# Performance work log

Measured on AMD Instinct MI355X. Metric: run time of the kernel, lower is better.

Reference implementation:

```python
import jax, jax.numpy as jnp
import numpy as np

HEADS = 8
DIM_HEAD = 128
LN_EPS = 1e-5


def setup_inputs() -> dict:
    key = jax.random.key(0)
    ks = jax.random.split(key, 4)
    N, M, C, V, T = 64, 2, 64, 15, 256
    dim = C * V              # 960
    inner = HEADS * DIM_HEAD # 1024
    return {
        "x": jax.random.normal(ks[0], (N, M, C, V, T), dtype=jnp.float32),
        "ln_g": jnp.ones((dim,), jnp.float32),
        "ln_b": jnp.zeros((dim,), jnp.float32),
        "w_qkv": jax.random.normal(ks[1], (dim, 3 * inner), dtype=jnp.float32) * (dim ** -0.5),
        "w_out": jax.random.normal(ks[2], (inner, dim), dtype=jnp.float32) * (inner ** -0.5),
        "b_out": jnp.zeros((dim,), jnp.float32),
        "w_lin": jax.random.normal(ks[3], (T, T), dtype=jnp.float32) * (T ** -0.5),
        "b_lin": jnp.zeros((T,), jnp.float32),
    }


def reference(x, ln_g, ln_b, w_qkv, w_out, b_out, w_lin, b_lin):
    N, M, C, V, T = x.shape
    dim = C * V
    # [N, M, C, V, T] -> [N*M, T, C*V]
    xs = jnp.transpose(x, (0, 1, 4, 2, 3)).reshape(N * M, T, dim)

    # PreNorm (LayerNorm over last dim)
    mu = jnp.mean(xs, axis=-1, keepdims=True)
    var = jnp.mean(jnp.square(xs - mu), axis=-1, keepdims=True)
    xn = (xs - mu) * jax.lax.rsqrt(var + LN_EPS) * ln_g + ln_b

    # Attention
    qkv = xn @ w_qkv  # [NM, T, 3*inner]
    q, k, v = jnp.split(qkv, 3, axis=-1)
    def to_heads(t):
        return jnp.transpose(t.reshape(N * M, T, HEADS, DIM_HEAD), (0, 2, 1, 3))
    q, k, v = to_heads(q), to_heads(k), to_heads(v)  # [NM, H, T, D]
    scale = DIM_HEAD ** -0.5
    dots = jnp.einsum('nhid,nhjd->nhij', q, k) * scale
    attn = jax.nn.softmax(dots, axis=-1)
    out = jnp.einsum('nhij,nhjd->nhid', attn, v)
    out = jnp.transpose(out, (0, 2, 1, 3)).reshape(N * M, T, HEADS * DIM_HEAD)
    out = out @ w_out + b_out

    # Residual
    xs = out + xs

    # back to [N, M, C, V, T], then Linear over T + tanh
    x2 = jnp.transpose(xs.reshape(N, M, T, C, V), (0, 1, 3, 4, 2))
    y = jnp.tanh(x2 @ w_lin.T + b_lin)
    return y
```

## Files before the change

kernel.cpp:

```cpp
#include <hip/hip_runtime.h>

typedef unsigned short ushort;
using short8 = __attribute__((ext_vector_type(8))) short;
using f32x4  = __attribute__((ext_vector_type(4))) float;
using i32x4  = __attribute__((ext_vector_type(4))) int;
using us4    = __attribute__((ext_vector_type(4))) ushort;

static __device__ __forceinline__ float bf2f(ushort u) {
  union { unsigned int i; float f; } x; x.i = ((unsigned int)u) << 16; return x.f;
}
static __device__ __forceinline__ ushort f2bf(float f) {
  union { float f; unsigned int i; } x; x.f = f;
  unsigned int u = x.i;
  unsigned int r = u + 0x7fffu + ((u >> 16) & 1u);
  return (ushort)(r >> 16);
}

#define GLOAD16(gp, lp)                                                   \
  __builtin_amdgcn_global_load_lds(                                      \
      (const __attribute__((address_space(1))) void*)(gp),               \
      (__attribute__((address_space(3))) void*)(lp), 16, 0, 0)

__global__ __launch_bounds__(256) void wtrans_kernel(const float* __restrict__ in,
                                                     ushort* __restrict__ out,
                                                     int R, int C) {
  __shared__ float sl[32][33];
  int tx = threadIdx.x & 31, ty = threadIdx.x >> 5;
  int c0 = blockIdx.x * 32, r0 = blockIdx.y * 32;
#pragma unroll
  for (int s = 0; s < 4; s++) {
    int r = r0 + ty + s * 8;
    int c = c0 + tx;
    sl[ty + s * 8][tx] = (c < C) ? in[(size_t)r * C + c] : 0.f;
  }
  __syncthreads();
#pragma unroll
  for (int s = 0; s < 4; s++) {
    int c = c0 + ty + s * 8;
    int r = r0 + tx;
    out[(size_t)c * R + r] = f2bf(sl[tx][ty + s * 8]);
  }
}

__global__ void wsplit_kernel(const float* __restrict__ in, ushort* __restrict__ hi,
                              ushort* __restrict__ lo, int n) {
  int i = blockIdx.x * 256 + threadIdx.x;
  if (i < n) {
    float v = in[i];
    ushort h = f2bf(v);
    hi[i] = h;
    lo[i] = f2bf(v - bf2f(h));
  }
}

__global__ __launch_bounds__(256) void ln_fused_kernel(const float* __restrict__ x,
                                                       const float* __restrict__ g,
                                                       const float* __restrict__ b,
                                                       ushort* __restrict__ xn) {
  __shared__ float sl[960][20];
  __shared__ float smean[16], srstd[16];
  int tid = threadIdx.x;
  int nm = blockIdx.y;
  int t0 = blockIdx.x * 16;

  int r0 = tid >> 2, c4 = (tid & 3) * 4;
#pragma unroll
  for (int it = 0; it < 15; it++) {
    int r = it * 64 + r0;
    float4 v = *(const float4*)&x[((size_t)nm * 960 + r) * 256 + t0 + c4];
    *(float4*)&sl[r][c4] = v;
  }
  __syncthreads();

  int tg = tid >> 4, lt = tid & 15;
  float s = 0.f, ss = 0.f;
#pragma unroll 4
  for (int k = 0; k < 60; k++) {
    float v = sl[lt + k * 16][tg];
    s += v; ss += v * v;
  }
#pragma unroll
  for (int d = 1; d < 16; d <<= 1) {
    s += __shfl_xor(s, d, 64);
    ss += __shfl_xor(ss, d, 64);
  }
  if (lt == 0) {
    float mean = s * (1.f / 960.f);
    float var = ss * (1.f / 960.f) - mean * mean;
    smean[tg] = mean;
    srstd[tg] = rsqrtf(var + 1e-5f);
  }
  __syncthreads();

  float gg[4], bb[4];
#pragma unroll
  for (int c = 0; c < 4; c++) {
    int col = c * 256 + tid;
    if (col < 960) { gg[c] = g[col]; bb[c] = b[col]; }
  }
#pragma unroll
  for (int t = 0; t < 16; t++) {
    float mean = smean[t], rstd = srstd[t];
#pragma unroll
    for (int c = 0; c < 4; c++) {
      int col = c * 256 + tid;
      if (col < 960)
        xn[((size_t)nm * 256 + t0 + t) * 960 + col] =
            f2bf((sl[col][t] - mean) * rstd * gg[c] + bb[c]);
    }
  }
}

template <int MODE>
__global__ __launch_bounds__(512, 2) void gemm256(
    const ushort* __restrict__ A, int lda, const ushort* __restrict__ BT, int ldb, int nkt,
    const ushort* __restrict__ Alo, const ushort* __restrict__ Blo,
    ushort* __restrict__ o0, ushort* __restrict__ o1, ushort* __restrict__ o2,
    const float* __restrict__ bias, float* __restrict__ fout) {
  __shared__ char smem[131072];
  int tid = threadIdx.x;
  int l = tid & 63, w = tid >> 6;
  int wr = w >> 2, wc = w & 3;
  int lr = l & 15, lg = l >> 4;
  int cb = blockIdx.x * 256, rb = blockIdx.y * 256;

  int srow = tid >> 2;
  int scol = ((tid & 3) ^ ((tid >> 3) & 3)) * 8;

  int swz = (lg ^ ((lr >> 1) & 3)) << 4;
  const char* ArdB = smem + (wr * 128 + lr) * 64 + swz;
  const char* BrdB = smem + 65536 + (wc * 64 + lr) * 64 + swz;

  auto stage_half = [&](int kt, int kk, int isB) {
    const ushort* P; int ld; int k0;
    if (MODE == 2) {
      int seg = kt >> 2; k0 = (kt & 3) * 64 + kk * 32;
      P = isB ? ((seg == 1) ? Blo : BT) : ((seg == 2) ? Alo : A);
      ld = 256;
    } else {
      P = isB ? BT : A; ld = isB ? ldb : lda; k0 = kt * 64 + kk * 32;
    }
    const ushort* gp = P + (size_t)((isB ? cb : rb) + srow) * ld + k0 + scol;
    char* dst = smem + isB * 65536 + (kt & 1) * 32768 + kk * 16384 + tid * 16;
    GLOAD16(gp, dst);
    GLOAD16(gp + (size_t)128 * ld, dst + 8192);
  };

  f32x4 acc[8][4];
#pragma unroll
  for (int i = 0; i < 8; i++)
#pragma unroll
    for (int j = 0; j < 4; j++) acc[i][j] = (f32x4){0.f, 0.f, 0.f, 0.f};

  stage_half(0, 0, 0); stage_half(0, 0, 1); stage_half(0, 1, 0); stage_half(0, 1, 1);
  asm volatile("s_waitcnt vmcnt(4)" ::: "memory");
  __builtin_amdgcn_s_barrier();

  for (int t = 0; t < nkt; t++) {
    const char* Ard = ArdB + (t & 1) * 32768;
    const char* Brd = BrdB + (t & 1) * 32768;
    bool st = (t + 1 < nkt);
    short8 a[4], b[4];

#pragma unroll
    for (int j = 0; j < 4; j++) b[j] = *(const short8*)(Brd + j * 1024);
#pragma unroll
    for (int i = 0; i < 4; i++) a[i] = *(const short8*)(Ard + i * 1024);
    if (st) stage_half(t + 1, 0, 0);
    __builtin_amdgcn_s_barrier();
    __builtin_amdgcn_s_setprio(1);
#pragma unroll
    for (int i = 0; i < 4; i++)
#pragma unroll
      for (int j = 0; j < 4; j++)
        acc[i][j] = __builtin_amdgcn_mfma_f32_16x16x32_bf16(a[i], b[j], acc[i][j], 0, 0, 0);
    __builtin_amdgcn_s_setprio(0);
    __builtin_amdgcn_s_barrier();

#pragma unroll
    for (int i = 0; i < 4; i++) a[i] = *(const short8*)(Ard + (4 + i) * 1024);
    if (st) stage_half(t + 1, 0, 1);
    __builtin_amdgcn_s_barrier();
    __builtin_amdgcn_s_setprio(1);
#pragma unroll
    for (int i = 0; i < 4; i++)
#pragma unroll
      for (int j = 0; j < 4; j++)
        acc[4 + i][j] = __builtin_amdgcn_mfma_f32_16x16x32_bf16(a[i], b[j], acc[4 + i][j], 0, 0, 0);
    __builtin_amdgcn_s_setprio(0);
    if (st) asm volatile("s_waitcnt vmcnt(4)" ::: "memory");
    else    asm volatile("s_waitcnt vmcnt(0)" ::: "memory");
    __builtin_amdgcn_s_barrier();

#pragma unroll
    for (int j = 0; j < 4; j++) b[j] = *(const short8*)(Brd + 16384 + j * 1024);
#pragma unroll
    for (int i = 0; i < 4; i++) a[i] = *(const short8*)(Ard + 16384 + i * 1024);
    if (st) stage_half(t + 1, 1, 0);
    __builtin_amdgcn_s_barrier();
    __builtin_amdgcn_s_setprio(1);
#pragma unroll
    for (int i = 0; i < 4; i++)
#pragma unroll
      for (int j = 0; j < 4; j++)
        acc[i][j] = __builtin_amdgcn_mfma_f32_16x16x32_bf16(a[i], b[j], acc[i][j], 0, 0, 0);
    __builtin_amdgcn_s_setprio(0);
    __builtin_amdgcn_s_barrier();

#pragma unroll
    for (int i = 0; i < 4; i++) a[i] = *(const short8*)(Ard + 16384 + (4 + i) * 1024);
    if (st) stage_half(t + 1, 1, 1);
    __builtin_amdgcn_s_barrier();
    __builtin_amdgcn_s_setprio(1);
#pragma unroll
    for (int i = 0; i < 4; i++)
#pragma unroll
      for (int j = 0; j < 4; j++)
        acc[4 + i][j] = __builtin_amdgcn_mfma_f32_16x16x32_bf16(a[i], b[j], acc[4 + i][j], 0, 0, 0);
    __builtin_amdgcn_s_setprio(0);
    if (st) asm volatile("s_waitcnt vmcnt(4)" ::: "memory");
    else    asm volatile("s_waitcnt vmcnt(0)" ::: "memory");
    __builtin_amdgcn_s_barrier();
  }

  int row0 = rb + wr * 128, col0 = cb + wc * 64;
  if (MODE == 0) {
    int nm = rb >> 8;
    int which = cb >> 10;
#pragma unroll
    for (int i = 0; i < 8; i++)
#pragma unroll
      for (int j = 0; j < 4; j++) {
        f32x4 v = acc[i][j];
        int col = col0 + j * 16 + lr;
        int cl = col & 1023;
        int h = cl >> 7, d = cl & 127;
        int nmh = nm * 8 + h;
        int t0 = wr * 128 + i * 16 + lg * 4;
        if (which == 2) {
          us4 pk;
          pk.x = f2bf(v[0]); pk.y = f2bf(v[1]); pk.z = f2bf(v[2]); pk.w = f2bf(v[3]);
          *(us4*)&o2[((size_t)nmh * 128 + d) * 256 + t0] = pk;
        } else if (which == 0) {
#pragma unroll
          for (int r = 0; r < 4; r++)
            o0[((size_t)nmh * 256 + t0 + r) * 128 + d] = f2bf(v[r] * 0.08838834764831845f);
        } else {
#pragma unroll
          for (int r = 0; r < 4; r++)
            o1[((size_t)nmh * 256 + t0 + r) * 128 + d] = f2bf(v[r]);
        }
      }
  } else if (MODE == 1) {
#pragma unroll
    for (int i = 0; i < 8; i++)
#pragma unroll
      for (int j = 0; j < 4; j++) {
        f32x4 v = acc[i][j];
        int col = col0 + j * 16 + lr;
        float bb = (col < 960) ? bias[col] : 0.f;
#pragma unroll
        for (int r = 0; r < 4; r++) {
          int row = row0 + i * 16 + lg * 4 + r;
          o0[(size_t)row * 1024 + col] = f2bf(v[r] + bb);
        }
      }
  } else {
#pragma unroll
    for (int i = 0; i < 8; i++)
#pragma unroll
      for (int j = 0; j < 4; j++) {
        f32x4 v = acc[i][j];
        int col = col0 + j * 16 + lr;
        float bb = bias[col];
#pragma unroll
        for (int r = 0; r < 4; r++) {
          int row = row0 + i * 16 + lg * 4 + r;
          fout[(size_t)row * 256 + col] = tanhf(v[r] + bb);
        }
      }
  }
}

__global__ __launch_bounds__(256) void attn_kernel(const ushort* __restrict__ q,
                                                   const ushort* __restrict__ kb,
                                                   const ushort* __restrict__ vT,
                                                   ushort* __restrict__ ao) {
  __shared__ ushort KVs[128 * 72];
  __shared__ ushort Ps[64 * 264];
  int tid = threadIdx.x;
  int l = tid & 63, w = tid >> 6;
  int lr = l & 15, lg = l >> 4;
  int qb = blockIdx.x;
  int nmh = blockIdx.y;

  short8 aq[4];
  {
    const ushort* qp = q + ((size_t)nmh * 256 + qb * 64 + w * 16 + lr) * 128 + lg * 8;
#pragma unroll
    for (int kk = 0; kk < 4; kk++) aq[kk] = *(const short8*)(qp + kk * 32);
  }

  f32x4 s_acc[16];
#pragma unroll
  for (int f = 0; f < 16; f++) s_acc[f] = (f32x4){0.f, 0.f, 0.f, 0.f};

  for (int ct = 0; ct < 4; ct++) {
    __syncthreads();
#pragma unroll
    for (int u = 0; u < 4; u++) {
      int i = tid + u * 256;
      int r = i >> 4, c = i & 15;
      *(i32x4*)&KVs[r * 136 + c * 8] =
          *(const i32x4*)(kb + ((size_t)nmh * 256 + ct * 64 + r) * 128 + c * 8);
    }
    __syncthreads();
#pragma unroll
    for (int j = 0; j < 4; j++) {
      short8 bk[4];
#pragma unroll
      for (int kk = 0; kk < 4; kk++)
        bk[kk] = *(const short8*)&KVs[(j * 16 + lr) * 136 + kk * 32 + lg * 8];
#pragma unroll
      for (int kk = 0; kk < 4; kk++)
        s_acc[ct * 4 + j] =
            __builtin_amdgcn_mfma_f32_16x16x32_bf16(aq[kk], bk[kk], s_acc[ct * 4 + j], 0, 0, 0);
    }
  }

  float m[4] = {-1e30f, -1e30f, -1e30f, -1e30f};
#pragma unroll
  for (int f = 0; f < 16; f++)
#pragma unroll
    for (int r = 0; r < 4; r++) m[r] = fmaxf(m[r], s_acc[f][r]);
#pragma unroll
  for (int dd = 1; dd < 16; dd <<= 1)
#pragma unroll
    for (int r = 0; r < 4; r++) m[r] = fmaxf(m[r], __shfl_xor(m[r], dd, 64));
  float sum[4] = {0.f, 0.f, 0.f, 0.f};
#pragma unroll
  for (int f = 0; f < 16; f++)
#pragma unroll
    for (int r = 0; r < 4; r++) {
      float p = __expf(s_acc[f][r] - m[r]);
      s_acc[f][r] = p;
      sum[r] += p;
    }
#pragma unroll
  for (int dd = 1; dd < 16; dd <<= 1)
#pragma unroll
    for (int r = 0; r < 4; r++) sum[r] += __shfl_xor(sum[r], dd, 64);
  float rs[4];
#pragma unroll
  for (int r = 0; r < 4; r++) rs[r] = 1.f / sum[r];

#pragma unroll
  for (int f = 0; f < 16; f++)
#pragma unroll
    for (int r = 0; r < 4; r++)
      Ps[(w * 16 + lg * 4 + r) * 264 + f * 16 + lr] = f2bf(s_acc[f][r]);

  f32x4 o_acc[8];
#pragma unroll
  for (int j = 0; j < 8; j++) o_acc[j] = (f32x4){0.f, 0.f, 0.f, 0.f};

  for (int ct = 0; ct < 4; ct++) {
    __syncthreads();
#pragma unroll
    for (int u = 0; u < 4; u++) {
      int i = tid + u * 256;
      int r = i >> 3, c = i & 7;
      *(i32x4*)&KVs[r * 72 + c * 8] =
          *(const i32x4*)(vT + ((size_t)nmh * 128 + r) * 256 + ct * 64 + c * 8);
    }
    __syncthreads();
#pragma unroll
    for (int kk = 0; kk < 2; kk++) {
      short8 ap = *(const short8*)&Ps[(w * 16 + lr) * 264 + ct * 64 + kk * 32 + lg * 8];
#pragma unroll
      for (int j = 0; j < 8; j++) {
        short8 bv = *(const short8*)&KVs[(j * 16 + lr) * 72 + kk * 32 + lg * 8];
        o_acc[j] = __builtin_amdgcn_mfma_f32_16x16x32_bf16(ap, bv, o_acc[j], 0, 0, 0);
      }
    }
  }

  int nm = nmh >> 3, h = nmh & 7;
  int trow0 = qb * 64 + w * 16;
#pragma unroll
  for (int j = 0; j < 8; j++)
#pragma unroll
    for (int r = 0; r < 4; r++) {
      int t = trow0 + lg * 4 + r;
      int d = h * 128 + j * 16 + lr;
      ao[((size_t)nm * 256 + t) * 1024 + d] = f2bf(o_acc[j][r] * rs[r]);
    }
}

__global__ __launch_bounds__(256) void x2split_kernel(const float* __restrict__ x,
                                                      const ushort* __restrict__ proj,
                                                      ushort* __restrict__ hi,
                                                      ushort* __restrict__ lo) {
  __shared__ ushort sl[64][65];
  int nm = blockIdx.y;
  int tb = blockIdx.x & 3, cvb = blockIdx.x >> 2;
  int t0 = tb * 64, cv0 = cvb * 64;
  int tx = threadIdx.x & 63, ty = threadIdx.x >> 6;
#pragma unroll
  for (int s = 0; s < 16; s++) {
    int r = ty + s * 4;
    sl[r][tx] = proj[((size_t)nm * 256 + t0 + r) * 1024 + cv0 + tx];
  }
  __syncthreads();
#pragma unroll
  for (int s = 0; s < 16; s++) {
    int cvl = ty + s * 4;
    size_t R = (size_t)nm * 960 + cv0 + cvl;
    float v = x[R * 256 + t0 + tx] + bf2f(sl[tx][cvl]);
    ushort h = f2bf(v);
    hi[R * 256 + t0 + tx] = h;
    lo[R * 256 + t0 + tx] = f2bf(v - bf2f(h));
  }
}

extern "C" void kernel_launch(void* const* d_in, const int* in_sizes, int n_in,
                              void* d_out, int out_size, void* d_ws, size_t ws_size,
                              hipStream_t stream) {
  const float* x = (const float*)d_in[0];
  const float* ln_g = (const float*)d_in[1];
  const float* ln_b = (const float*)d_in[2];
  const float* w_qkv = (const float*)d_in[3];
  const float* w_out = (const float*)d_in[4];
  const float* b_out = (const float*)d_in[5];
  const float* w_lin = (const float*)d_in[6];
  const float* b_lin = (const float*)d_in[7];
  float* out = (float*)d_out;

  char* ws = (char*)d_ws;
  size_t off = 0;
  auto alloc = [&](size_t bytes) -> void* {
    void* p = ws + off;
    off = (off + bytes + 255) & ~(size_t)255;
    return p;
  };

  ushort* wqkvT = (ushort*)alloc((size_t)3072 * 960 * 2);
  ushort* woutT = (ushort*)alloc((size_t)1024 * 1024 * 2);
  ushort* whi   = (ushort*)alloc((size_t)65536 * 2);
  ushort* wlo   = (ushort*)alloc((size_t)65536 * 2);
  ushort* xn    = (ushort*)alloc((size_t)32768 * 960 * 2);
  ushort* qbuf  = (ushort*)alloc((size_t)1024 * 256 * 128 * 2);
  ushort* kbuf  = (ushort*)alloc((size_t)1024 * 256 * 128 * 2);
  ushort* vTbuf = (ushort*)alloc((size_t)1024 * 256 * 128 * 2);
  ushort* attnout = (ushort*)alloc((size_t)32768 * 1024 * 2);
  ushort* proj = qbuf;
  ushort* x2hi = kbuf;
  ushort* x2lo = vTbuf;

  wtrans_kernel<<<dim3(96, 30), 256, 0, stream>>>(w_qkv, wqkvT, 960, 3072);
  wtrans_kernel<<<dim3(32, 32), 256, 0, stream>>>(w_out, woutT, 1024, 960);
  wsplit_kernel<<<dim3(256), 256, 0, stream>>>(w_lin, whi, wlo, 65536);

  ln_fused_kernel<<<dim3(16, 128), 256, 0, stream>>>(x, ln_g, ln_b, xn);

  gemm256<0><<<dim3(12, 128), 512, 0, stream>>>(xn, 960, wqkvT, 960, 15, nullptr, nullptr,
                                                qbuf, kbuf, vTbuf, nullptr, nullptr);
  attn_kernel<<<dim3(4, 1024), 256, 0, stream>>>(qbuf, kbuf, vTbuf, attnout);
  gemm256<1><<<dim3(4, 128), 512, 0, stream>>>(attnout, 1024, woutT, 1024, 16, nullptr, nullptr,
                                               proj, nullptr, nullptr, b_out, nullptr);
  x2split_kernel<<<dim3(60, 128), 256, 0, stream>>>(x, proj, x2hi, x2lo);
  gemm256<2><<<dim3(1, 480), 512, 0, stream>>>(x2hi, 256, whi, 256, 12, x2lo, wlo,
                                               nullptr, nullptr, nullptr, b_lin, out);
}
```

Before: 683.7 us.

## Process whole head per attention block and store projection transposed

The attention kernel now gives one 512-thread block a whole head. It loads all of K and V^T once into 128KB of swizzled LDS with async global-to-LDS loads, and each wave handles 32 query rows. This removes the 4x redundant K/V loads and the repeated barriers of the old per-64-row blocks. The out-projection GEMM epilogue writes its result transposed ([nm][cv][t]) as packed 4-element stores, so the residual/split kernel becomes a simple vectorized elementwise pass with no LDS transpose. The cost is fewer resident blocks per CU (large LDS), plus reliance on correct vmcnt waits and swizzle indexing.

```diff
diff --git a/kernel.cpp b/kernel.cpp
--- a/kernel.cpp
+++ b/kernel.cpp
@@ -252,6 +252,7 @@
         }
       }
   } else if (MODE == 1) {
+    int nm = rb >> 8;
 #pragma unroll
     for (int i = 0; i < 8; i++)
 #pragma unroll
@@ -259,11 +260,11 @@
         f32x4 v = acc[i][j];
         int col = col0 + j * 16 + lr;
         float bb = (col < 960) ? bias[col] : 0.f;
-#pragma unroll
-        for (int r = 0; r < 4; r++) {
-          int row = row0 + i * 16 + lg * 4 + r;
-          o0[(size_t)row * 1024 + col] = f2bf(v[r] + bb);
-        }
+        int t0 = wr * 128 + i * 16 + lg * 4;
+        us4 pk;
+        pk.x = f2bf(v[0] + bb); pk.y = f2bf(v[1] + bb);
+        pk.z = f2bf(v[2] + bb); pk.w = f2bf(v[3] + bb);
+        *(us4*)&o0[((size_t)nm * 1024 + col) * 256 + t0] = pk;
       }
   } else {
 #pragma unroll
@@ -282,145 +283,177 @@
   }
 }
 
-__global__ __launch_bounds__(256) void attn_kernel(const ushort* __restrict__ q,
-                                                   const ushort* __restrict__ kb,
-                                                   const ushort* __restrict__ vT,
-                                                   ushort* __restrict__ ao) {
-  __shared__ ushort KVs[128 * 72];
-  __shared__ ushort Ps[64 * 264];
+__global__ __launch_bounds__(512, 2) void attn2_kernel(const ushort* __restrict__ q,
+                                                       const ushort* __restrict__ kb,
+                                                       const ushort* __restrict__ vT,
+                                                       ushort* __restrict__ ao) {
+  __shared__ char smem[131072];
   int tid = threadIdx.x;
   int l = tid & 63, w = tid >> 6;
   int lr = l & 15, lg = l >> 4;
-  int qb = blockIdx.x;
-  int nmh = blockIdx.y;
-
-  short8 aq[4];
+  int nmh = blockIdx.x;
+
+  const ushort* kbase = kb + (size_t)nmh * 32768;
+  const ushort* vbase = vT + (size_t)nmh * 32768;
+
+#pragma unroll
+  for (int u = 0; u < 8; u++) {
+    int row = u * 32 + w * 4 + (l >> 4);
+    int slot = l & 15;
+    GLOAD16(kbase + row * 128 + ((slot ^ (row & 7)) * 8), smem + u * 8192 + w * 1024);
+  }
+  short8 aq[2][4];
   {
-    const ushort* qp = q + ((size_t)nmh * 256 + qb * 64 + w * 16 + lr) * 128 + lg * 8;
-#pragma unroll
-    for (int kk = 0; kk < 4; kk++) aq[kk] = *(const short8*)(qp + kk * 32);
-  }
-
-  f32x4 s_acc[16];
-#pragma unroll
-  for (int f = 0; f < 16; f++) s_acc[f] = (f32x4){0.f, 0.f, 0.f, 0.f};
-
+    const ushort* qp = q + (size_t)nmh * 32768 + (size_t)(w * 32 + lr) * 128 + lg * 8;
+#pragma unroll
+    for (int i = 0; i < 2; i++)
+#pragma unroll
+      for (int kk = 0; kk < 4; kk++) aq[i][kk] = *(const short8*)(qp + i * 2048 + kk * 32);
+  }
+#pragma unroll
+  for (int u = 0; u < 8; u++) {
+    int row = u * 16 + w * 2 + (l >> 5);
+    int slot = l & 31;
+    GLOAD16(vbase + row * 256 + ((slot ^ (row & 7)) * 8),
+            smem + 65536 + u * 8192 + w * 1024);
+  }
+  asm volatile("s_waitcnt vmcnt(8)" ::: "memory");
+  __builtin_amdgcn_s_barrier();
+
+  f32x4 s_acc[2][16];
+#pragma unroll
+  for (int i = 0; i < 2; i++)
+#pragma unroll
+    for (int j = 0; j < 16; j++) s_acc[i][j] = (f32x4){0.f, 0.f, 0.f, 0.f};
+#pragma unroll
+  for (int j = 0; j < 16; j++) {
+    short8 bk[4];
+#pragma unroll
+    for (int kk = 0; kk < 4; kk++)
+      bk[kk] = *(const short8*)(smem + (j * 16 + lr) * 256 + (((kk * 4 + lg) ^ (lr & 7)) << 4));
+#pragma unroll
+    for (int i = 0; i < 2; i++)
+#pragma unroll
+      for (int kk = 0; kk < 4; kk++)
+        s_acc[i][j] = __builtin_amdgcn_mfma_f32_16x16x32_bf16(aq[i][kk], bk[kk], s_acc[i][j], 0, 0, 0);
+  }
+
+  float m[2][4], sum[2][4], rs[2][4];
+#pragma unroll
+  for (int i = 0; i < 2; i++)
+#pragma unroll
+    for (int r = 0; r < 4; r++) m[i][r] = -1e30f;
+#pragma unroll
+  for (int i = 0; i < 2; i++)
+#pragma unroll
+    for (int j = 0; j < 16; j++)
+#pragma unroll
+      for (int r = 0; r < 4; r++) m[i][r] = fmaxf(m[i][r], s_acc[i][j][r]);
+#pragma unroll
+  for (int d = 1; d < 16; d <<= 1)
+#pragma unroll
+    for (int i = 0; i < 2; i++)
+#pragma unroll
+      for (int r = 0; r < 4; r++) m[i][r] = fmaxf(m[i][r], __shfl_xor(m[i][r], d, 64));
+#pragma unroll
+  for (int i = 0; i < 2; i++)
+#pragma unroll
+    for (int r = 0; r < 4; r++) sum[i][r] = 0.f;
+#pragma unroll
+  for (int i = 0; i < 2; i++)
+#pragma unroll
+    for (int j = 0; j < 16; j++)
+#pragma unroll
+      for (int r = 0; r < 4; r++) {
+        float p = __expf(s_acc[i][j][r] - m[i][r]);
+        s_acc[i][j][r] = p;
+        sum[i][r] += p;
+      }
+#pragma unroll
+  for (int d = 1; d < 16; d <<= 1)
+#pragma unroll
+    for (int i = 0; i < 2; i++)
+#pragma unroll
+      for (int r = 0; r < 4; r++) sum[i][r] += __shfl_xor(sum[i][r], d, 64);
+#pragma unroll
+  for (int i = 0; i < 2; i++)
+#pragma unroll
+    for (int r = 0; r < 4; r++) rs[i][r] = 1.f / sum[i][r];
+
+  __builtin_amdgcn_s_barrier();
+  asm volatile("s_waitcnt vmcnt(0)" ::: "memory");
+
+  char* Pb = smem + w * 4608;
+  f32x4 o_acc[2][8];
+#pragma unroll
+  for (int i = 0; i < 2; i++)
+#pragma unroll
+    for (int j = 0; j < 8; j++) o_acc[i][j] = (f32x4){0.f, 0.f, 0.f, 0.f};
+
+#pragma unroll
   for (int ct = 0; ct < 4; ct++) {
-    __syncthreads();
-#pragma unroll
-    for (int u = 0; u < 4; u++) {
-      int i = tid + u * 256;
-      int r = i >> 4, c = i & 15;
-      *(i32x4*)&KVs[r * 136 + c * 8] =
-          *(const i32x4*)(kb + ((size_t)nmh * 256 + ct * 64 + r) * 128 + c * 8);
+#pragma unroll
+    for (int i = 0; i < 2; i++)
+#pragma unroll
+      for (int jj = 0; jj < 4; jj++)
+#pragma unroll
+        for (int r = 0; r < 4; r++)
+          *(ushort*)(Pb + (i * 16 + lg * 4 + r) * 144 + (jj * 16 + lr) * 2) =
+              f2bf(s_acc[i][ct * 4 + jj][r]);
+    short8 pa[2][2];
+#pragma unroll
+    for (int i = 0; i < 2; i++)
+#pragma unroll
+      for (int kk = 0; kk < 2; kk++)
+        pa[i][kk] = *(const short8*)(Pb + (i * 16 + lr) * 144 + kk * 64 + lg * 16);
+#pragma unroll
+    for (int j = 0; j < 8; j++) {
+      short8 bv[2];
+#pragma unroll
+      for (int kk = 0; kk < 2; kk++)
+        bv[kk] = *(const short8*)(smem + 65536 + (j * 16 + lr) * 512 +
+                                  (((ct * 8 + kk * 4 + lg) ^ (lr & 7)) << 4));
+#pragma unroll
+      for (int i = 0; i < 2; i++)
+#pragma unroll
+        for (int kk = 0; kk < 2; kk++)
+          o_acc[i][j] = __builtin_amdgcn_mfma_f32_16x16x32_bf16(pa[i][kk], bv[kk], o_acc[i][j], 0, 0, 0);
     }
-    __syncthreads();
-#pragma unroll
-    for (int j = 0; j < 4; j++) {
-      short8 bk[4];
-#pragma unroll
-      for (int kk = 0; kk < 4; kk++)
-        bk[kk] = *(const short8*)&KVs[(j * 16 + lr) * 136 + kk * 32 + lg * 8];
-#pragma unroll
-      for (int kk = 0; kk < 4; kk++)
-        s_acc[ct * 4 + j] =
-            __builtin_amdgcn_mfma_f32_16x16x32_bf16(aq[kk], bk[kk], s_acc[ct * 4 + j], 0, 0, 0);
-    }
-  }
-
-  float m[4] = {-1e30f, -1e30f, -1e30f, -1e30f};
-#pragma unroll
-  for (int f = 0; f < 16; f++)
-#pragma unroll
-    for (int r = 0; r < 4; r++) m[r] = fmaxf(m[r], s_acc[f][r]);
-#pragma unroll
-  for (int dd = 1; dd < 16; dd <<= 1)
-#pragma unroll
-    for (int r = 0; r < 4; r++) m[r] = fmaxf(m[r], __shfl_xor(m[r], dd, 64));
-  float sum[4] = {0.f, 0.f, 0.f, 0.f};
-#pragma unroll
-  for (int f = 0; f < 16; f++)
-#pragma unroll
-    for (int r = 0; r < 4; r++) {
-      float p = __expf(s_acc[f][r] - m[r]);
-      s_acc[f][r] = p;
-      sum[r] += p;
-    }
-#pragma unroll
-  for (int dd = 1; dd < 16; dd <<= 1)
-#pragma unroll
-    for (int r = 0; r < 4; r++) sum[r] += __shfl_xor(sum[r], dd, 64);
-  float rs[4];
-#pragma unroll
-  for (int r = 0; r < 4; r++) rs[r] = 1.f / sum[r];
-
-#pragma unroll
-  for (int f = 0; f < 16; f++)
-#pragma unroll
-    for (int r = 0; r < 4; r++)
-      Ps[(w * 16 + lg * 4 + r) * 264 + f * 16 + lr] = f2bf(s_acc[f][r]);
-
-  f32x4 o_acc[8];
-#pragma unroll
-  for (int j = 0; j < 8; j++) o_acc[j] = (f32x4){0.f, 0.f, 0.f, 0.f};
-
-  for (int ct = 0; ct < 4; ct++) {
-    __syncthreads();
-#pragma unroll
-    for (int u = 0; u < 4; u++) {
-      int i = tid + u * 256;
-      int r = i >> 3, c = i & 7;
-      *(i32x4*)&KVs[r * 72 + c * 8] =
-          *(const i32x4*)(vT + ((size_t)nmh * 128 + r) * 256 + ct * 64 + c * 8);
-    }
-    __syncthreads();
-#pragma unroll
-    for (int kk = 0; kk < 2; kk++) {
-      short8 ap = *(const short8*)&Ps[(w * 16 + lr) * 264 + ct * 64 + kk * 32 + lg * 8];
-#pragma unroll
-      for (int j = 0; j < 8; j++) {
-        short8 bv = *(const short8*)&KVs[(j * 16 + lr) * 72 + kk * 32 + lg * 8];
-        o_acc[j] = __builtin_amdgcn_mfma_f32_16x16x32_bf16(ap, bv, o_acc[j], 0, 0, 0);
+  }
+
+  int nm = nmh >> 3, h = nmh & 7;
+#pragma unroll
+  for (int i = 0; i < 2; i++)
+#pragma unroll
+    for (int j = 0; j < 8; j++)
+#pragma unroll
+      for (int r = 0; r < 4; r++) {
+        int t = w * 32 + i * 16 + lg * 4 + r;
+        int d = h * 128 + j * 16 + lr;
+        ao[((size_t)nm * 256 + t) * 1024 + d] = f2bf(o_acc[i][j][r] * rs[i][r]);
       }
-    }
-  }
-
-  int nm = nmh >> 3, h = nmh & 7;
-  int trow0 = qb * 64 + w * 16;
-#pragma unroll
-  for (int j = 0; j < 8; j++)
-#pragma unroll
-    for (int r = 0; r < 4; r++) {
-      int t = trow0 + lg * 4 + r;
-      int d = h * 128 + j * 16 + lr;
-      ao[((size_t)nm * 256 + t) * 1024 + d] = f2bf(o_acc[j][r] * rs[r]);
-    }
 }
 
 __global__ __launch_bounds__(256) void x2split_kernel(const float* __restrict__ x,
-                                                      const ushort* __restrict__ proj,
+                                                      const ushort* __restrict__ projT,
                                                       ushort* __restrict__ hi,
                                                       ushort* __restrict__ lo) {
-  __shared__ ushort sl[64][65];
   int nm = blockIdx.y;
-  int tb = blockIdx.x & 3, cvb = blockIdx.x >> 2;
-  int t0 = tb * 64, cv0 = cvb * 64;
-  int tx = threadIdx.x & 63, ty = threadIdx.x >> 6;
-#pragma unroll
-  for (int s = 0; s < 16; s++) {
-    int r = ty + s * 4;
-    sl[r][tx] = proj[((size_t)nm * 256 + t0 + r) * 1024 + cv0 + tx];
-  }
-  __syncthreads();
-#pragma unroll
-  for (int s = 0; s < 16; s++) {
-    int cvl = ty + s * 4;
-    size_t R = (size_t)nm * 960 + cv0 + cvl;
-    float v = x[R * 256 + t0 + tx] + bf2f(sl[tx][cvl]);
-    ushort h = f2bf(v);
-    hi[R * 256 + t0 + tx] = h;
-    lo[R * 256 + t0 + tx] = f2bf(v - bf2f(h));
-  }
+  int cv = blockIdx.x * 4 + (threadIdx.x >> 6);
+  int t = (threadIdx.x & 63) * 4;
+  size_t xi = ((size_t)nm * 960 + cv) * 256 + t;
+  f32x4 xv = *(const f32x4*)&x[xi];
+  us4 pv = *(const us4*)&projT[((size_t)nm * 1024 + cv) * 256 + t];
+  us4 h, lo4;
+#pragma unroll
+  for (int e = 0; e < 4; e++) {
+    float s = xv[e] + bf2f(pv[e]);
+    ushort hh = f2bf(s);
+    h[e] = hh;
+    lo4[e] = f2bf(s - bf2f(hh));
+  }
+  *(us4*)&hi[xi] = h;
+  *(us4*)&lo[xi] = lo4;
 }
 
 extern "C" void kernel_launch(void* const* d_in, const int* in_sizes, int n_in,
@@ -453,9 +486,9 @@
   ushort* kbuf  = (ushort*)alloc((size_t)1024 * 256 * 128 * 2);
   ushort* vTbuf = (ushort*)alloc((size_t)1024 * 256 * 128 * 2);
   ushort* attnout = (ushort*)alloc((size_t)32768 * 1024 * 2);
-  ushort* proj = qbuf;
-  ushort* x2hi = kbuf;
-  ushort* x2lo = vTbuf;
+  ushort* projT = qbuf;
+  ushort* x2hi  = kbuf;
+  ushort* x2lo  = vTbuf;
 
   wtrans_kernel<<<dim3(96, 30), 256, 0, stream>>>(w_qkv, wqkvT, 960, 3072);
   wtrans_kernel<<<dim3(32, 32), 256, 0, stream>>>(w_out, woutT, 1024, 960);
@@ -465,10 +498,10 @@
 
   gemm256<0><<<dim3(12, 128), 512, 0, stream>>>(xn, 960, wqkvT, 960, 15, nullptr, nullptr,
                                                 qbuf, kbuf, vTbuf, nullptr, nullptr);
-  attn_kernel<<<dim3(4, 1024), 256, 0, stream>>>(qbuf, kbuf, vTbuf, attnout);
+  attn2_kernel<<<dim3(1024), 512, 0, stream>>>(qbuf, kbuf, vTbuf, attnout);
   gemm256<1><<<dim3(4, 128), 512, 0, stream>>>(attnout, 1024, woutT, 1024, 16, nullptr, nullptr,
-                                               proj, nullptr, nullptr, b_out, nullptr);
-  x2split_kernel<<<dim3(60, 128), 256, 0, stream>>>(x, proj, x2hi, x2lo);
+                                               projT, nullptr, nullptr, b_out, nullptr);
+  x2split_kernel<<<dim3(240, 128), 256, 0, stream>>>(x, projT, x2hi, x2lo);
   gemm256<2><<<dim3(1, 480), 512, 0, stream>>>(x2hi, 256, whi, 256, 12, x2lo, wlo,
                                                nullptr, nullptr, nullptr, b_lin, out);
 }
```

Result: faster. 622.8 us (median of 2 runs) (-8.9%).
